# Performance work log

Measured on AMD Instinct MI355X. Metric: run time of the kernel, lower is better.

Reference implementation:

```python
import jax, jax.numpy as jnp
import numpy as np

N_NODES = 10000
N_EDGES = 640000
D_FEAT = 128


def setup_inputs() -> dict:
    key = jax.random.key(0)
    k1, k2, k3, k4 = jax.random.split(key, 4)
    feat = jax.random.normal(k1, (N_NODES, D_FEAT), dtype=jnp.float32)
    src = jax.random.randint(k2, (N_EDGES,), 0, N_NODES, dtype=jnp.int32)
    dst = jax.random.randint(k3, (N_EDGES,), 0, N_NODES, dtype=jnp.int32)
    W = jax.random.normal(k4, (D_FEAT, D_FEAT), dtype=jnp.float32) / np.sqrt(D_FEAT).astype(np.float32)
    b = jnp.zeros((D_FEAT,), dtype=jnp.float32)
    return {"feat": feat, "W": W, "b": b, "src": src, "dst": dst}


def reference(feat, W, b, src, dst):
    eps = jnp.float32(0.0)  # init_eps=0, learn_eps=False (buffer)
    n = feat.shape[0]
    # message passing: copy_u('h','m') + sum reducer -> neigh[i] = sum_{j->i} h_j
    h_src = feat[src]                                   # [E, D] gather
    neigh = jax.ops.segment_sum(h_src, dst, num_segments=n)  # [N, D] scatter-add
    rst = (1.0 + eps) * feat + neigh
    # apply_func: Linear(D, D)
    rst = rst @ W + b
    # per-edge score: e = sum(h_src * tanh(h_dst), axis=1)
    e = jnp.sum(h_src * jnp.tanh(feat[dst]), axis=1)    # [E]
    # edge_softmax: softmax over edges grouped by destination node
    m = jax.ops.segment_max(e, dst, num_segments=n)     # [N]
    e_exp = jnp.exp(e - m[dst])
    denom = jax.ops.segment_sum(e_exp, dst, num_segments=n)  # [N]
    e_soft = e_exp / denom[dst]
    return rst, e_soft
```

## Files before the change

kernel.cpp:

```cpp
#include <hip/hip_runtime.h>
#include <hip/hip_bf16.h>
#include <math.h>

#define N_NODES 10000
#define N_EDGES 640000
#define D_FEAT  128
#define SLOT    128
#define MAXDEG  128


__device__ __forceinline__ unsigned bf16rne2(float a, float b) {
    unsigned ua = __float_as_uint(a);
    unsigned ub = __float_as_uint(b);
    unsigned ra = (ua + 0x7fffu + ((ua >> 16) & 1u)) >> 16;
    unsigned rb = (ub + 0x7fffu + ((ub >> 16) & 1u)) >> 16;
    return ra | (rb << 16);
}

__global__ void scatter_build(const int* __restrict__ src,
                              const int* __restrict__ dst,
                              const float* __restrict__ feat,
                              int* __restrict__ cnt,
                              unsigned short* __restrict__ slot_us,
                              int* __restrict__ pos_by_edge,
                              unsigned short* __restrict__ feat_bf) {
    int tid = blockIdx.x * 256 + threadIdx.x;

    {
        int t8 = tid * 8;
        float4 f0 = *(const float4*)&feat[t8];
        float4 f1 = *(const float4*)&feat[t8 + 4];
        uint4 p;
        p.x = bf16rne2(f0.x, f0.y);
        p.y = bf16rne2(f0.z, f0.w);
        p.z = bf16rne2(f1.x, f1.y);
        p.w = bf16rne2(f1.z, f1.w);
        *(uint4*)&feat_bf[t8] = p;
    }

    int i0 = tid * 4;
    int4 s4 = *(const int4*)&src[i0];
    int4 d4 = *(const int4*)&dst[i0];
    int p0 = atomicAdd(&cnt[d4.x << 4], 1);
    int p1 = atomicAdd(&cnt[d4.y << 4], 1);
    int p2 = atomicAdd(&cnt[d4.z << 4], 1);
    int p3 = atomicAdd(&cnt[d4.w << 4], 1);
    int4 q;
    q.x = d4.x * SLOT + p0;
    q.y = d4.y * SLOT + p1;
    q.z = d4.z * SLOT + p2;
    q.w = d4.w * SLOT + p3;
    slot_us[q.x] = (unsigned short)s4.x;
    slot_us[q.y] = (unsigned short)s4.y;
    slot_us[q.z] = (unsigned short)s4.z;
    slot_us[q.w] = (unsigned short)s4.w;
    *(int4*)&pos_by_edge[i0] = q;
}

__device__ __forceinline__ float cvt_acc_dot(uint4 U, float4 t0, float4 t1,
                                             float4& a0, float4& a1) {
    float v0 = __uint_as_float(U.x << 16);
    float v1 = __uint_as_float(U.x & 0xffff0000u);
    float v2 = __uint_as_float(U.y << 16);
    float v3 = __uint_as_float(U.y & 0xffff0000u);
    float v4 = __uint_as_float(U.z << 16);
    float v5 = __uint_as_float(U.z & 0xffff0000u);
    float v6 = __uint_as_float(U.w << 16);
    float v7 = __uint_as_float(U.w & 0xffff0000u);
    a0.x += v0; a0.y += v1; a0.z += v2; a0.w += v3;
    a1.x += v4; a1.y += v5; a1.z += v6; a1.w += v7;
    return v0 * t0.x + v1 * t0.y + v2 * t0.z + v3 * t0.w
         + v4 * t1.x + v5 * t1.y + v6 * t1.z + v7 * t1.w;
}

__global__ void fused_node(const float* __restrict__ feat,
                           const unsigned short* __restrict__ feat_bf,
                           const int* __restrict__ cnt,
                           const unsigned short* __restrict__ slot_us,
                           float* __restrict__ e_slot,
                           float* __restrict__ x_out) {
    __shared__ float t_sh[4][D_FEAT];
    __shared__ float e_sh[4][MAXDEG];
    int wv = threadIdx.x >> 6;
    int lane = threadIdx.x & 63;
    int node = blockIdx.x * 4 + wv;
    if (node >= N_NODES) return;

    int g = lane >> 4;
    int l = lane & 15;

    int deg = cnt[node << 4];
    int dm = (deg > 0) ? deg - 1 : 0;
    unsigned base = (unsigned)node * SLOT;

    float2 fd2 = ((const float2*)(feat + (size_t)node * D_FEAT))[lane];
    ((float2*)&t_sh[wv][0])[lane] = make_float2(tanhf(fd2.x), tanhf(fd2.y));
    float4 t0 = ((const float4*)&t_sh[wv][0])[l * 2];
    float4 t1 = ((const float4*)&t_sh[wv][0])[l * 2 + 1];

    int m0 = (int)slot_us[base + min(lane, dm)];
    int m1 = (int)slot_us[base + min(64 + lane, dm)];

    float4 acc0 = make_float4(0.f, 0.f, 0.f, 0.f);
    float4 acc1 = make_float4(0.f, 0.f, 0.f, 0.f);

    int nsteps = (deg + 7) >> 3;

    uint4 Ua0, Ua1;
    #define LOAD_STEP(T, U0, U1)                                              \
        {                                                                     \
            int m_ = ((T) < 8) ? m0 : m1;                                     \
            int s0_ = __shfl(m_, ((T) * 8 + g) & 63, 64);                     \
            int s1_ = __shfl(m_, ((T) * 8 + 4 + g) & 63, 64);                 \
            U0 = *((const uint4*)(feat_bf + (size_t)s0_ * D_FEAT) + l);       \
            U1 = *((const uint4*)(feat_bf + (size_t)s1_ * D_FEAT) + l);       \
        }

    if (nsteps > 0) LOAD_STEP(0, Ua0, Ua1);

    for (int t = 0; t < nsteps; ++t) {
        uint4 Ub0 = Ua0, Ub1 = Ua1;
        if (t + 1 < nsteps) LOAD_STEP(t + 1, Ub0, Ub1);

        int i0 = t * 8 + g;
        int i1 = i0 + 4;
        if (((t + 1) << 3) <= deg) {
            float d0 = cvt_acc_dot(Ua0, t0, t1, acc0, acc1);
            float d1 = cvt_acc_dot(Ua1, t0, t1, acc0, acc1);
            #pragma unroll
            for (int off = 1; off <= 8; off <<= 1) {
                d0 += __shfl_xor(d0, off, 64);
                d1 += __shfl_xor(d1, off, 64);
            }
            if (l == 0) {
                e_sh[wv][i0] = d0;
                e_sh[wv][i1] = d1;
            }
        } else {
            bool a0 = i0 < deg, a1 = i1 < deg;
            if (!a0) Ua0 = make_uint4(0u, 0u, 0u, 0u);
            if (!a1) Ua1 = make_uint4(0u, 0u, 0u, 0u);
            float d0 = cvt_acc_dot(Ua0, t0, t1, acc0, acc1);
            float d1 = cvt_acc_dot(Ua1, t0, t1, acc0, acc1);
            #pragma unroll
            for (int off = 1; off <= 8; off <<= 1) {
                d0 += __shfl_xor(d0, off, 64);
                d1 += __shfl_xor(d1, off, 64);
            }
            if (a0 && l == 0) e_sh[wv][i0] = d0;
            if (a1 && l == 0) e_sh[wv][i1] = d1;
        }
        Ua0 = Ub0; Ua1 = Ub1;
    }
    #undef LOAD_STEP

    #pragma unroll
    for (int off = 16; off <= 32; off <<= 1) {
        acc0.x += __shfl_xor(acc0.x, off, 64);
        acc0.y += __shfl_xor(acc0.y, off, 64);
        acc0.z += __shfl_xor(acc0.z, off, 64);
        acc0.w += __shfl_xor(acc0.w, off, 64);
        acc1.x += __shfl_xor(acc1.x, off, 64);
        acc1.y += __shfl_xor(acc1.y, off, 64);
        acc1.z += __shfl_xor(acc1.z, off, 64);
        acc1.w += __shfl_xor(acc1.w, off, 64);
    }

    float2 mp = (g == 0) ? make_float2(acc0.x, acc0.y)
              : (g == 1) ? make_float2(acc0.z, acc0.w)
              : (g == 2) ? make_float2(acc1.x, acc1.y)
              :            make_float2(acc1.z, acc1.w);
    int p2 = l * 4 + g;
    float2 fn = ((const float2*)(feat + (size_t)node * D_FEAT))[p2];
    ((float2*)(x_out + (size_t)node * D_FEAT))[p2] =
        make_float2(mp.x + fn.x, mp.y + fn.y);

    float mx = -INFINITY;
    for (int i = lane; i < deg; i += 64) mx = fmaxf(mx, e_sh[wv][i]);
    #pragma unroll
    for (int off = 32; off; off >>= 1)
        mx = fmaxf(mx, __shfl_xor(mx, off, 64));

    float sum = 0.f;
    for (int i = lane; i < deg; i += 64) {
        float ex = expf(e_sh[wv][i] - mx);
        e_sh[wv][i] = ex;
        sum += ex;
    }
    #pragma unroll
    for (int off = 32; off; off >>= 1)
        sum += __shfl_xor(sum, off, 64);

    float inv = 1.0f / sum;
    for (int i = lane; i < deg; i += 64)
        e_slot[base + i] = e_sh[wv][i] * inv;
}

__global__ void gemm_and_edge(float* __restrict__ io,
                              const float* __restrict__ W,
                              const float* __restrict__ b,
                              const int* __restrict__ pos_by_edge,
                              const float* __restrict__ e_slot,
                              float* __restrict__ out_e) {
    if (blockIdx.x >= 625) {
        int i4 = ((blockIdx.x - 625) * 256 + threadIdx.x) * 4;
        int4 p = *(const int4*)&pos_by_edge[i4];
        float4 r;
        r.x = e_slot[p.x];
        r.y = e_slot[p.y];
        r.z = e_slot[p.z];
        r.w = e_slot[p.w];
        *(float4*)&out_e[i4] = r;
        return;
    }

    __shared__ float xst[D_FEAT][20];
    int rbase = blockIdx.x * 16;

    for (int i = threadIdx.x; i < 16 * D_FEAT; i += 256) {
        int r = i >> 7, c = i & 127;
        xst[c][r] = io[(size_t)(rbase + r) * D_FEAT + c];
    }
    __syncthreads();

    int tc = threadIdx.x & 63;
    int rh = threadIdx.x >> 6;
    float a00 = 0.f, a01 = 0.f, a10 = 0.f, a11 = 0.f;
    float a20 = 0.f, a21 = 0.f, a30 = 0.f, a31 = 0.f;

    for (int k = 0; k < D_FEAT; ++k) {
        float2 xa = *(const float2*)&xst[k][rh * 4];
        float2 xb = *(const float2*)&xst[k][rh * 4 + 2];
        float2 w  = *(const float2*)&W[(size_t)k * D_FEAT + tc * 2];
        a00 += xa.x * w.x; a01 += xa.x * w.y;
        a10 += xa.y * w.x; a11 += xa.y * w.y;
        a20 += xb.x * w.x; a21 += xb.x * w.y;
        a30 += xb.y * w.x; a31 += xb.y * w.y;
    }
    __syncthreads();

    float2 bias = *(const float2*)&b[tc * 2];
    int rw = rbase + rh * 4;
    ((float2*)&io[(size_t)(rw + 0) * D_FEAT])[tc] = make_float2(a00 + bias.x, a01 + bias.y);
    ((float2*)&io[(size_t)(rw + 1) * D_FEAT])[tc] = make_float2(a10 + bias.x, a11 + bias.y);
    ((float2*)&io[(size_t)(rw + 2) * D_FEAT])[tc] = make_float2(a20 + bias.x, a21 + bias.y);
    ((float2*)&io[(size_t)(rw + 3) * D_FEAT])[tc] = make_float2(a30 + bias.x, a31 + bias.y);
}

extern "C" void kernel_launch(void* const* d_in, const int* in_sizes, int n_in,
                              void* d_out, int out_size, void* d_ws, size_t ws_size,
                              hipStream_t stream) {
    const float* feat = (const float*)d_in[0];
    const float* W    = (const float*)d_in[1];
    const float* b    = (const float*)d_in[2];
    const int*   src  = (const int*)d_in[3];
    const int*   dst  = (const int*)d_in[4];

    float* out_rst = (float*)d_out;
    float* out_e   = (float*)d_out + (size_t)N_NODES * D_FEAT;

    char* ws = (char*)d_ws;
    int*            cnt         = (int*)(ws + 0);
    unsigned short* slot_us     = (unsigned short*)(ws + 640000);
    float*          e_slot      = (float*)(ws + 3200000);
    int*            pos_by_edge = (int*)(ws + 8320000);
    unsigned short* feat_bf     = (unsigned short*)(ws + 10880000);

    hipMemsetAsync(cnt, 0, 640000, stream);

    scatter_build<<<N_EDGES / 4 / 256, 256, 0, stream>>>(src, dst, feat, cnt,
                                                         slot_us, pos_by_edge, feat_bf);

    fused_node<<<(N_NODES + 3) / 4, 256, 0, stream>>>(feat, feat_bf, cnt,
                                                      slot_us, e_slot, out_rst);

    gemm_and_edge<<<1250, 256, 0, stream>>>(out_rst, W, b, pos_by_edge, e_slot, out_e);
}
```

Before: 137.5 us.

## Store edge ids in slots, scatter softmax directly, and deepen gather prefetch

The bucketing kernel now stores the edge id in each destination slot instead of the source id and no longer writes a position-by-edge array. The node kernel looks up src through that edge id and writes each normalized softmax value straight to its original edge position. This removes the intermediate e_slot buffer and the separate edge-permutation pass from the GEMM kernel. The feature-gather loop also keeps four steps of loads in flight instead of one, at the cost of more registers and an extra indirection through src.

Result: slower. 146.3 us (+6.4%).

```diff
diff --git a/kernel.cpp b/kernel.cpp
--- a/kernel.cpp
+++ b/kernel.cpp
@@ -17,12 +17,10 @@
     return ra | (rb << 16);
 }
 
-__global__ void scatter_build(const int* __restrict__ src,
-                              const int* __restrict__ dst,
+__global__ void scatter_build(const int* __restrict__ dst,
                               const float* __restrict__ feat,
                               int* __restrict__ cnt,
-                              unsigned short* __restrict__ slot_us,
-                              int* __restrict__ pos_by_edge,
+                              unsigned* __restrict__ slot_u,
                               unsigned short* __restrict__ feat_bf) {
     int tid = blockIdx.x * 256 + threadIdx.x;
 
@@ -39,22 +37,15 @@
     }
 
     int i0 = tid * 4;
-    int4 s4 = *(const int4*)&src[i0];
     int4 d4 = *(const int4*)&dst[i0];
     int p0 = atomicAdd(&cnt[d4.x << 4], 1);
     int p1 = atomicAdd(&cnt[d4.y << 4], 1);
     int p2 = atomicAdd(&cnt[d4.z << 4], 1);
     int p3 = atomicAdd(&cnt[d4.w << 4], 1);
-    int4 q;
-    q.x = d4.x * SLOT + p0;
-    q.y = d4.y * SLOT + p1;
-    q.z = d4.z * SLOT + p2;
-    q.w = d4.w * SLOT + p3;
-    slot_us[q.x] = (unsigned short)s4.x;
-    slot_us[q.y] = (unsigned short)s4.y;
-    slot_us[q.z] = (unsigned short)s4.z;
-    slot_us[q.w] = (unsigned short)s4.w;
-    *(int4*)&pos_by_edge[i0] = q;
+    slot_u[d4.x * SLOT + p0] = (unsigned)(i0 + 0);
+    slot_u[d4.y * SLOT + p1] = (unsigned)(i0 + 1);
+    slot_u[d4.z * SLOT + p2] = (unsigned)(i0 + 2);
+    slot_u[d4.w * SLOT + p3] = (unsigned)(i0 + 3);
 }
 
 __device__ __forceinline__ float cvt_acc_dot(uint4 U, float4 t0, float4 t1,
@@ -75,9 +66,10 @@
 
 __global__ void fused_node(const float* __restrict__ feat,
                            const unsigned short* __restrict__ feat_bf,
+                           const int* __restrict__ src,
                            const int* __restrict__ cnt,
-                           const unsigned short* __restrict__ slot_us,
-                           float* __restrict__ e_slot,
+                           const unsigned* __restrict__ slot_u,
+                           float* __restrict__ out_e,
                            float* __restrict__ x_out) {
     __shared__ float t_sh[4][D_FEAT];
     __shared__ float e_sh[4][MAXDEG];
@@ -98,15 +90,16 @@
     float4 t0 = ((const float4*)&t_sh[wv][0])[l * 2];
     float4 t1 = ((const float4*)&t_sh[wv][0])[l * 2 + 1];
 
-    int m0 = (int)slot_us[base + min(lane, dm)];
-    int m1 = (int)slot_us[base + min(64 + lane, dm)];
+    unsigned e0id = slot_u[base + min(lane, dm)];
+    unsigned e1id = slot_u[base + min(64 + lane, dm)];
+    int m0 = src[min(e0id, (unsigned)(N_EDGES - 1))];
+    int m1 = src[min(e1id, (unsigned)(N_EDGES - 1))];
 
     float4 acc0 = make_float4(0.f, 0.f, 0.f, 0.f);
     float4 acc1 = make_float4(0.f, 0.f, 0.f, 0.f);
 
     int nsteps = (deg + 7) >> 3;
 
-    uint4 Ua0, Ua1;
     #define LOAD_STEP(T, U0, U1)                                              \
         {                                                                     \
             int m_ = ((T) < 8) ? m0 : m1;                                     \
@@ -116,43 +109,62 @@
             U1 = *((const uint4*)(feat_bf + (size_t)s1_ * D_FEAT) + l);       \
         }
 
-    if (nsteps > 0) LOAD_STEP(0, Ua0, Ua1);
-
-    for (int t = 0; t < nsteps; ++t) {
-        uint4 Ub0 = Ua0, Ub1 = Ua1;
-        if (t + 1 < nsteps) LOAD_STEP(t + 1, Ub0, Ub1);
-
-        int i0 = t * 8 + g;
-        int i1 = i0 + 4;
-        if (((t + 1) << 3) <= deg) {
-            float d0 = cvt_acc_dot(Ua0, t0, t1, acc0, acc1);
-            float d1 = cvt_acc_dot(Ua1, t0, t1, acc0, acc1);
-            #pragma unroll
-            for (int off = 1; off <= 8; off <<= 1) {
-                d0 += __shfl_xor(d0, off, 64);
-                d1 += __shfl_xor(d1, off, 64);
-            }
-            if (l == 0) {
-                e_sh[wv][i0] = d0;
-                e_sh[wv][i1] = d1;
-            }
-        } else {
-            bool a0 = i0 < deg, a1 = i1 < deg;
-            if (!a0) Ua0 = make_uint4(0u, 0u, 0u, 0u);
-            if (!a1) Ua1 = make_uint4(0u, 0u, 0u, 0u);
-            float d0 = cvt_acc_dot(Ua0, t0, t1, acc0, acc1);
-            float d1 = cvt_acc_dot(Ua1, t0, t1, acc0, acc1);
-            #pragma unroll
-            for (int off = 1; off <= 8; off <<= 1) {
-                d0 += __shfl_xor(d0, off, 64);
-                d1 += __shfl_xor(d1, off, 64);
-            }
-            if (a0 && l == 0) e_sh[wv][i0] = d0;
-            if (a1 && l == 0) e_sh[wv][i1] = d1;
-        }
-        Ua0 = Ub0; Ua1 = Ub1;
+    #define PROC_STEP(T, U0, U1)                                              \
+        {                                                                     \
+            int i0_ = (T) * 8 + g;                                            \
+            int i1_ = i0_ + 4;                                                \
+            if ((((T) + 1) << 3) <= deg) {                                    \
+                float d0 = cvt_acc_dot(U0, t0, t1, acc0, acc1);               \
+                float d1 = cvt_acc_dot(U1, t0, t1, acc0, acc1);               \
+                _Pragma("unroll")                                             \
+                for (int off = 1; off <= 8; off <<= 1) {                      \
+                    d0 += __shfl_xor(d0, off, 64);                            \
+                    d1 += __shfl_xor(d1, off, 64);                            \
+                }                                                             \
+                if (l == 0) {                                                 \
+                    e_sh[wv][i0_] = d0;                                       \
+                    e_sh[wv][i1_] = d1;                                       \
+                }                                                             \
+            } else {                                                          \
+                bool a0_ = i0_ < deg, a1_ = i1_ < deg;                        \
+                if (!a0_) U0 = make_uint4(0u, 0u, 0u, 0u);                    \
+                if (!a1_) U1 = make_uint4(0u, 0u, 0u, 0u);                    \
+                float d0 = cvt_acc_dot(U0, t0, t1, acc0, acc1);               \
+                float d1 = cvt_acc_dot(U1, t0, t1, acc0, acc1);               \
+                _Pragma("unroll")                                             \
+                for (int off = 1; off <= 8; off <<= 1) {                      \
+                    d0 += __shfl_xor(d0, off, 64);                            \
+                    d1 += __shfl_xor(d1, off, 64);                            \
+                }                                                             \
+                if (a0_ && l == 0) e_sh[wv][i0_] = d0;                        \
+                if (a1_ && l == 0) e_sh[wv][i1_] = d1;                        \
+            }                                                                 \
+        }
+
+    uint4 A0, A1, B0, B1, C0, C1, D0, D1;
+    if (nsteps > 0) LOAD_STEP(0, A0, A1);
+    if (nsteps > 1) LOAD_STEP(1, B0, B1);
+    if (nsteps > 2) LOAD_STEP(2, C0, C1);
+    if (nsteps > 3) LOAD_STEP(3, D0, D1);
+
+    for (int t = 0; t < nsteps; t += 4) {
+        PROC_STEP(t, A0, A1);
+        if (t + 4 < nsteps) LOAD_STEP(t + 4, A0, A1);
+        if (t + 1 < nsteps) {
+            PROC_STEP(t + 1, B0, B1);
+            if (t + 5 < nsteps) LOAD_STEP(t + 5, B0, B1);
+        }
+        if (t + 2 < nsteps) {
+            PROC_STEP(t + 2, C0, C1);
+            if (t + 6 < nsteps) LOAD_STEP(t + 6, C0, C1);
+        }
+        if (t + 3 < nsteps) {
+            PROC_STEP(t + 3, D0, D1);
+            if (t + 7 < nsteps) LOAD_STEP(t + 7, D0, D1);
+        }
     }
     #undef LOAD_STEP
+    #undef PROC_STEP
 
     #pragma unroll
     for (int off = 16; off <= 32; off <<= 1) {
@@ -192,28 +204,13 @@
         sum += __shfl_xor(sum, off, 64);
 
     float inv = 1.0f / sum;
-    for (int i = lane; i < deg; i += 64)
-        e_slot[base + i] = e_sh[wv][i] * inv;
-}
-
-__global__ void gemm_and_edge(float* __restrict__ io,
-                              const float* __restrict__ W,
-                              const float* __restrict__ b,
-                              const int* __restrict__ pos_by_edge,
-                              const float* __restrict__ e_slot,
-                              float* __restrict__ out_e) {
-    if (blockIdx.x >= 625) {
-        int i4 = ((blockIdx.x - 625) * 256 + threadIdx.x) * 4;
-        int4 p = *(const int4*)&pos_by_edge[i4];
-        float4 r;
-        r.x = e_slot[p.x];
-        r.y = e_slot[p.y];
-        r.z = e_slot[p.z];
-        r.w = e_slot[p.w];
-        *(float4*)&out_e[i4] = r;
-        return;
-    }
-
+    if (lane < deg)      out_e[e0id] = e_sh[wv][lane] * inv;
+    if (64 + lane < deg) out_e[e1id] = e_sh[wv][64 + lane] * inv;
+}
+
+__global__ void node_gemm(float* __restrict__ io,
+                          const float* __restrict__ W,
+                          const float* __restrict__ b) {
     __shared__ float xst[D_FEAT][20];
     int rbase = blockIdx.x * 16;
 
@@ -260,19 +257,16 @@
     float* out_e   = (float*)d_out + (size_t)N_NODES * D_FEAT;
 
     char* ws = (char*)d_ws;
-    int*            cnt         = (int*)(ws + 0);
-    unsigned short* slot_us     = (unsigned short*)(ws + 640000);
-    float*          e_slot      = (float*)(ws + 3200000);
-    int*            pos_by_edge = (int*)(ws + 8320000);
-    unsigned short* feat_bf     = (unsigned short*)(ws + 10880000);
+    int*            cnt     = (int*)(ws + 0);
+    unsigned*       slot_u  = (unsigned*)(ws + 640000);
+    unsigned short* feat_bf = (unsigned short*)(ws + 5760000);
 
     hipMemsetAsync(cnt, 0, 640000, stream);
 
-    scatter_build<<<N_EDGES / 4 / 256, 256, 0, stream>>>(src, dst, feat, cnt,
-                                                         slot_us, pos_by_edge, feat_bf);
-
-    fused_node<<<(N_NODES + 3) / 4, 256, 0, stream>>>(feat, feat_bf, cnt,
-                                                      slot_us, e_slot, out_rst);
-
-    gemm_and_edge<<<1250, 256, 0, stream>>>(out_rst, W, b, pos_by_edge, e_slot, out_e);
-}
+    scatter_build<<<N_EDGES / 4 / 256, 256, 0, stream>>>(dst, feat, cnt, slot_u, feat_bf);
+
+    fused_node<<<(N_NODES + 3) / 4, 256, 0, stream>>>(feat, feat_bf, src, cnt,
+                                                      slot_u, out_e, out_rst);
+
+    node_gemm<<<N_NODES / 16, 256, 0, stream>>>(out_rst, W, b);
+}
```
